# Kernel tuning notes

Measured on AMD Instinct MI355X. Metric: run time of the kernel, lower is better.

## Reference

```python
import jax, jax.numpy as jnp
import numpy as np


def setup_inputs() -> dict:
    key = jax.random.key(0)
    kx, kq, kk, kv = jax.random.split(key, 4)
    d_model, d_head = 1024, 64
    x = jax.random.normal(kx, (4, 4096, d_model), dtype=jnp.float32)
    scale = 1.0 / np.sqrt(d_model)
    Wq = jax.random.normal(kq, (d_model, d_head), dtype=jnp.float32) * scale
    Wk = jax.random.normal(kk, (d_model, d_head), dtype=jnp.float32) * scale
    Wv = jax.random.normal(kv, (d_model, d_head), dtype=jnp.float32) * scale
    return {"x": x, "Wq": Wq, "Wk": Wk, "Wv": Wv}


def reference(x, Wq, Wk, Wv):
    # x: [B, S, D]; Wq/Wk/Wv: [D, H]
    d_head = Wq.shape[-1]
    Q = jnp.einsum('bsd,dh->bsh', x, Wq)
    K = jnp.einsum('bsd,dh->bsh', x, Wk)
    V = jnp.einsum('bsd,dh->bsh', x, Wv)
    scores = jnp.einsum('bqh,bkh->bqk', Q, K) / jnp.sqrt(jnp.float32(d_head))
    S = x.shape[1]
    causal = jnp.tril(jnp.ones((S, S), dtype=bool))  # [S, S]
    scores = jnp.where(causal, scores, -jnp.inf)
    weights = jax.nn.softmax(scores, axis=-1)  # [B, S, S]
    return jnp.einsum('bqk,bkh->bqh', weights, V)
```

## Files before the change

kernel.cpp:

```cpp
#include <hip/hip_runtime.h>

#define D_MODEL 1024
#define D_HEAD  64
#define SEQ     4096
#define BATCH   4
#define M_TOT   (BATCH * SEQ)
#define LOG2E   1.44269504088896f
#define MFIX_L2 17.3123404906676f
#define CHUNK   8

typedef __bf16 bf16;
typedef bf16  bf16x8 __attribute__((ext_vector_type(8)));
typedef bf16  bf16x4v __attribute__((ext_vector_type(4)));
typedef float f32x4  __attribute__((ext_vector_type(4)));

#define MFMA(a, b, c) __builtin_amdgcn_mfma_f32_16x16x32_bf16(a, b, c, 0, 0, 0)

#define QKV_OFF  0
#define OBUF_OFF 6291456
#define LBUF_OFF 10485760
#define WT_OFF   10551296
#define VT_OFF   10944512

__global__ void prep_kernel(const float* __restrict__ Wq, const float* __restrict__ Wk,
                            const float* __restrict__ Wv, bf16* __restrict__ Wt,
                            float4* __restrict__ zp, int n4)
{
    const int bx = blockIdx.x;
    const int t  = threadIdx.x;
    if (bx < 48) {
        __shared__ bf16 tr[64][72];
        const int wm = bx >> 4, kt = bx & 15, k0 = kt * 64;
        const float* W = (wm == 0) ? Wq : (wm == 1) ? Wk : Wv;
        const int kr = t >> 2, nb = (t & 3) * 16;
        #pragma unroll
        for (int j = 0; j < 4; j++) {
            float4 wrow = *(const float4*)(W + (size_t)(k0 + kr) * D_HEAD + nb + j * 4);
            tr[nb + j * 4 + 0][kr] = (bf16)wrow.x;
            tr[nb + j * 4 + 1][kr] = (bf16)wrow.y;
            tr[nb + j * 4 + 2][kr] = (bf16)wrow.z;
            tr[nb + j * 4 + 3][kr] = (bf16)wrow.w;
        }
        __syncthreads();
        const int n = t >> 2, kc = (t & 3) * 8;
        bf16* dst = Wt + (size_t)(wm * 64 + n) * D_MODEL + k0;
        #pragma unroll
        for (int h = 0; h < 2; h++) {
            bf16x8 v;
            #pragma unroll
            for (int j = 0; j < 8; j++) v[j] = tr[n][kc + h * 32 + j];
            *(bf16x8*)(dst + kc + h * 32) = v;
        }
    } else {
        int i = (bx - 48) * 256 + t;
        if (i < n4) zp[i] = float4{0.f, 0.f, 0.f, 0.f};
    }
}

#define XP 40

__global__ __launch_bounds__(512) void proj_kernel(
    const float* __restrict__ x, const bf16* __restrict__ Wt,
    bf16* __restrict__ qkv, bf16* __restrict__ vt)
{
    __shared__ __align__(16) bf16 xs[2][2][64][XP];
    __shared__ __align__(16) bf16 ws[2][2][192][XP];
    __shared__ float red[64][193];

    const int t    = threadIdx.x;
    const int w    = t >> 6;
    const int g    = w >> 2;
    const int nw   = w & 3;
    const int lane = t & 63;
    const int quad = lane >> 4;
    const int l15  = lane & 15;
    const int row0 = blockIdx.x * 64;
    const int kb   = g * 512;

    const int tg   = t & 255;
    const int xrow = tg >> 2, xkq = (tg & 3) * 8;

    const float* xg = x + (size_t)(row0 + xrow) * D_MODEL + kb + xkq;

    f32x4 acc[12] = {};

    float4 xa, xb;
    bf16x8 wtv[3];

    auto load_regs = [&](int c) {
        xa = *(const float4*)(xg + c * 32);
        xb = *(const float4*)(xg + c * 32 + 4);
        #pragma unroll
        for (int it = 0; it < 3; it++) {
            int id = tg + it * 256, n = id >> 2, kk8 = (id & 3) * 8;
            wtv[it] = *(const bf16x8*)(Wt + (size_t)n * D_MODEL + kb + c * 32 + kk8);
        }
    };
    auto store_lds = [&](int p) {
        bf16x8 xv;
        xv[0] = (bf16)xa.x; xv[1] = (bf16)xa.y; xv[2] = (bf16)xa.z; xv[3] = (bf16)xa.w;
        xv[4] = (bf16)xb.x; xv[5] = (bf16)xb.y; xv[6] = (bf16)xb.z; xv[7] = (bf16)xb.w;
        *(bf16x8*)&xs[p][g][xrow][xkq] = xv;
        #pragma unroll
        for (int it = 0; it < 3; it++) {
            int id = tg + it * 256, n = id >> 2, kk8 = (id & 3) * 8;
            *(bf16x8*)&ws[p][g][n][kk8] = wtv[it];
        }
    };

    load_regs(0);
    store_lds(0);
    load_regs(1);
    __syncthreads();

    int p = 0;
    for (int c = 0; c < 16; c++) {
        bf16x8 af[4], bfr[3];
        #pragma unroll
        for (int rg = 0; rg < 4; rg++)
            af[rg] = *(bf16x8*)&xs[p][g][rg * 16 + l15][quad * 8];
        #pragma unroll
        for (int j = 0; j < 3; j++)
            bfr[j] = *(bf16x8*)&ws[p][g][nw * 48 + j * 16 + l15][quad * 8];
        #pragma unroll
        for (int rg = 0; rg < 4; rg++)
            #pragma unroll
            for (int j = 0; j < 3; j++)
                acc[rg * 3 + j] = MFMA(af[rg], bfr[j], acc[rg * 3 + j]);

        if (c + 1 < 16) {
            store_lds(p ^ 1);
            if (c + 2 < 16) load_regs(c + 2);
        }
        __syncthreads();
        p ^= 1;
    }

    if (g == 1) {
        #pragma unroll
        for (int rg = 0; rg < 4; rg++)
            #pragma unroll
            for (int j = 0; j < 3; j++)
                #pragma unroll
                for (int r = 0; r < 4; r++)
                    red[rg * 16 + quad * 4 + r][nw * 48 + j * 16 + l15] =
                        acc[rg * 3 + j][r];
    }
    __syncthreads();
    if (g == 0) {
        const int bb = row0 >> 12, s0 = row0 & (SEQ - 1);
        #pragma unroll
        for (int rg = 0; rg < 4; rg++)
            #pragma unroll
            for (int j = 0; j < 3; j++) {
                const int col = nw * 48 + j * 16 + l15;
                const int wm = col >> 6, h = col & 63;
                if (wm == 2) {
                    bf16x4v vv;
                    #pragma unroll
                    for (int r = 0; r < 4; r++) {
                        const int row = rg * 16 + quad * 4 + r;
                        vv[r] = (bf16)(acc[rg * 3 + j][r] + red[row][col]);
                    }
                    *(bf16x4v*)(vt + ((size_t)bb * D_HEAD + h) * SEQ +
                                s0 + rg * 16 + quad * 4) = vv;
                } else {
                    const float sc = (wm == 0) ? 0.125f : 1.0f;
                    bf16* outp = qkv + (size_t)wm * M_TOT * D_HEAD;
                    #pragma unroll
                    for (int r = 0; r < 4; r++) {
                        const int row = rg * 16 + quad * 4 + r;
                        float s = acc[rg * 3 + j][r] + red[row][col];
                        outp[(size_t)(row0 + row) * D_HEAD + h] = (bf16)(s * sc);
                    }
                }
            }
    }
}

__global__ __launch_bounds__(256, 4) void attn_kernel(
    const bf16* __restrict__ qkv, const bf16* __restrict__ vt,
    float* __restrict__ o_buf, float* __restrict__ l_buf)
{
    const int i = blockIdx.x;
    const int c = blockIdx.y;
    const int b = blockIdx.z;
    const int ntiles = i + 1;
    const int tile0  = c * CHUNK;
    if (tile0 >= ntiles) return;
    const int tile1 = min(tile0 + CHUNK, ntiles);

    __shared__ __align__(16) char KsB[2 * 64 * 128];
    __shared__ __align__(16) char VsB[2 * 64 * 128];

    auto kaddr = [](char* base, int pp, int row, int colb) -> void* {
        return base + pp * 8192 + row * 128 + (colb ^ ((row & 7) << 4));
    };

    const bf16* Q = qkv;
    const bf16* K = qkv + (size_t)M_TOT * D_HEAD;

    const int t    = threadIdx.x;
    const int wv   = t >> 6;
    const int lane = t & 63;
    const int quad = lane >> 4;
    const int l15  = lane & 15;
    const int qb   = i * 64;
    const size_t base  = (size_t)b * SEQ * D_HEAD;
    const bf16* vtb = vt + (size_t)b * D_HEAD * SEQ;

    bf16x8 qf0, qf1;
    {
        const bf16* qr = Q + base + (size_t)(qb + wv * 16 + l15) * D_HEAD;
        qf0 = *(const bf16x8*)(qr + quad * 8);
        qf1 = *(const bf16x8*)(qr + 32 + quad * 8);
    }

    f32x4 o[4] = {};
    float lsum = 0.f;
    const int qw0 = qb + wv * 16;

    const int dr  = t >> 2;
    const int cb  = (t & 3) * 16;

    bf16x8 kr0, kr1, vr0, vr1;
    auto load_kv = [&](int tile) {
        const bf16* kp = K + base + (size_t)(tile * 64 + dr) * D_HEAD;
        kr0 = *(const bf16x8*)(kp + (cb >> 1));
        kr1 = *(const bf16x8*)(kp + (cb >> 1) + 32);
        const bf16* vp = vtb + (size_t)dr * SEQ + tile * 64;
        vr0 = *(const bf16x8*)(vp + (cb >> 1));
        vr1 = *(const bf16x8*)(vp + (cb >> 1) + 32);
    };
    auto store_kv = [&](int pp) {
        *(bf16x8*)kaddr(KsB, pp, dr, cb)      = kr0;
        *(bf16x8*)kaddr(KsB, pp, dr, cb + 64) = kr1;
        *(bf16x8*)kaddr(VsB, pp, dr, cb)      = vr0;
        *(bf16x8*)kaddr(VsB, pp, dr, cb + 64) = vr1;
    };

    load_kv(tile0);
    store_kv(0);
    if (tile0 + 1 < tile1) load_kv(tile0 + 1);
    __syncthreads();

    int p = 0;
    for (int tile = tile0; tile < tile1; tile++) {
        const int kk0 = tile * 64;

        f32x4 sc4[4];
        __builtin_amdgcn_s_setprio(1);
        #pragma unroll
        for (int kt = 0; kt < 4; kt++) {
            f32x4 z = {};
            z = MFMA(*(bf16x8*)kaddr(KsB, p, kt * 16 + l15, quad * 16),      qf0, z);
            z = MFMA(*(bf16x8*)kaddr(KsB, p, kt * 16 + l15, 64 + quad * 16), qf1, z);
            sc4[kt] = z;
        }
        __builtin_amdgcn_s_setprio(0);

        bf16 ph[4][4];
        if (tile == i) {
            #pragma unroll
            for (int kt = 0; kt < 4; kt++)
                #pragma unroll
                for (int r = 0; r < 4; r++) {
                    float s = sc4[kt][r];
                    if (kk0 + kt * 16 + quad * 4 + r > qw0 + l15)
                        s = -1e30f;
                    float pe = __builtin_amdgcn_exp2f(fmaf(s, LOG2E, -MFIX_L2));
                    lsum += pe;
                    ph[kt][r] = (bf16)pe;
                }
        } else {
            #pragma unroll
            for (int kt = 0; kt < 4; kt++)
                #pragma unroll
                for (int r = 0; r < 4; r++) {
                    float pe = __builtin_amdgcn_exp2f(
                        fmaf(sc4[kt][r], LOG2E, -MFIX_L2));
                    lsum += pe;
                    ph[kt][r] = (bf16)pe;
                }
        }

        unsigned pku[4][2];
        #pragma unroll
        for (int kt = 0; kt < 4; kt++) {
            __builtin_memcpy(&pku[kt][0], &ph[kt][0], 4);
            __builtin_memcpy(&pku[kt][1], &ph[kt][2], 4);
        }

        const int srcA = l15 + ((lane & 16) ? 32 : 0);
        const int srcB = srcA + 16;
        const bool hi  = (lane & 32) != 0;

        #pragma unroll
        for (int c2 = 0; c2 < 2; c2++) {
            unsigned xA0 = __shfl((int)pku[2 * c2][0],     srcA);
            unsigned xA1 = __shfl((int)pku[2 * c2][1],     srcA);
            unsigned yA0 = __shfl((int)pku[2 * c2 + 1][0], srcA);
            unsigned yA1 = __shfl((int)pku[2 * c2 + 1][1], srcA);
            unsigned xB0 = __shfl((int)pku[2 * c2][0],     srcB);
            unsigned xB1 = __shfl((int)pku[2 * c2][1],     srcB);
            unsigned yB0 = __shfl((int)pku[2 * c2 + 1][0], srcB);
            unsigned yB1 = __shfl((int)pku[2 * c2 + 1][1], srcB);
            unsigned fr[4];
            fr[0] = hi ? yA0 : xA0;
            fr[1] = hi ? yA1 : xA1;
            fr[2] = hi ? yB0 : xB0;
            fr[3] = hi ? yB1 : xB1;
            bf16x8 pa;
            __builtin_memcpy(&pa, fr, 16);

            __builtin_amdgcn_s_setprio(1);
            #pragma unroll
            for (int t4 = 0; t4 < 4; t4++) {
                bf16x8 vb = *(bf16x8*)kaddr(VsB, p, t4 * 16 + l15,
                                            c2 * 64 + quad * 16);
                o[t4] = MFMA(pa, vb, o[t4]);
            }
            __builtin_amdgcn_s_setprio(0);
        }

        if (tile + 1 < tile1) {
            store_kv(p ^ 1);
            if (tile + 2 < tile1) load_kv(tile + 2);
            __syncthreads();
        }
        p ^= 1;
    }

    const int mrow0 = b * SEQ + qw0;
    lsum += __shfl_xor(lsum, 16, 64);
    lsum += __shfl_xor(lsum, 32, 64);
    if (lane < 16)
        atomicAdd(&l_buf[mrow0 + l15], lsum);
    #pragma unroll
    for (int r = 0; r < 4; r++) {
        const size_t orow = (size_t)(mrow0 + quad * 4 + r) * D_HEAD;
        #pragma unroll
        for (int t4 = 0; t4 < 4; t4++)
            atomicAdd(&o_buf[orow + t4 * 16 + l15], o[t4][r]);
    }
}

__global__ void norm_kernel(const float4* __restrict__ o_buf,
                            const float* __restrict__ l_buf,
                            float4* __restrict__ out)
{
    int gid = blockIdx.x * 256 + threadIdx.x;
    int m = gid >> 4;
    float inv = 1.0f / l_buf[m];
    float4 v = o_buf[gid];
    out[gid] = float4{v.x * inv, v.y * inv, v.z * inv, v.w * inv};
}

extern "C" void kernel_launch(void* const* d_in, const int* in_sizes, int n_in,
                              void* d_out, int out_size, void* d_ws, size_t ws_size,
                              hipStream_t stream) {
    const float* x  = (const float*)d_in[0];
    const float* Wq = (const float*)d_in[1];
    const float* Wk = (const float*)d_in[2];
    const float* Wv = (const float*)d_in[3];

    bf16*  qkv   = (bf16*)((char*)d_ws + QKV_OFF);
    float* o_buf = (float*)((char*)d_ws + OBUF_OFF);
    float* l_buf = (float*)((char*)d_ws + LBUF_OFF);
    bf16*  Wt    = (bf16*)((char*)d_ws + WT_OFF);
    bf16*  vt    = (bf16*)((char*)d_ws + VT_OFF);

    const int zero4 = (M_TOT * 65) / 4;
    const int zblocks = (zero4 + 255) / 256;
    prep_kernel<<<48 + zblocks, 256, 0, stream>>>(Wq, Wk, Wv, Wt,
                                                  (float4*)o_buf, zero4);
    proj_kernel<<<M_TOT / 64, 512, 0, stream>>>(x, Wt, qkv, vt);
    attn_kernel<<<dim3(SEQ / 64, SEQ / 64 / CHUNK, BATCH), 256, 0, stream>>>(
        qkv, vt, o_buf, l_buf);
    norm_kernel<<<M_TOT * 16 / 256, 256, 0, stream>>>((const float4*)o_buf, l_buf,
                                                      (float4*)d_out);
}
```

Measured before the change: 147.8 us.

## Drop split-K in projection, use 32-row tiles, and double attention chunk size

The projection kernel stops splitting the K dimension across two warp groups, which removes the LDS reduction buffer and the extra barrier. It now runs 256-thread blocks over 32-row tiles with a full 1024-wide K loop, giving twice as many blocks. Attention CHUNK grows from 8 to 16, so each block handles more KV tiles and fewer partial outputs get atomically accumulated. In exchange, weight reuse per block drops (each W tile is loaded for only 32 rows), and larger chunks may reduce attention parallelism and load balance.

```diff
diff --git a/kernel.cpp b/kernel.cpp
--- a/kernel.cpp
+++ b/kernel.cpp
@@ -7,7 +7,7 @@
 #define M_TOT   (BATCH * SEQ)
 #define LOG2E   1.44269504088896f
 #define MFIX_L2 17.3123404906676f
-#define CHUNK   8
+#define CHUNK   16
 
 typedef __bf16 bf16;
 typedef bf16  bf16x8 __attribute__((ext_vector_type(8)));
@@ -57,54 +57,47 @@
     }
 }
 
-#define XP 40
-
-__global__ __launch_bounds__(512) void proj_kernel(
+#define PXP 40
+
+__global__ __launch_bounds__(256) void proj_kernel(
     const float* __restrict__ x, const bf16* __restrict__ Wt,
     bf16* __restrict__ qkv, bf16* __restrict__ vt)
 {
-    __shared__ __align__(16) bf16 xs[2][2][64][XP];
-    __shared__ __align__(16) bf16 ws[2][2][192][XP];
-    __shared__ float red[64][193];
+    __shared__ __align__(16) bf16 xs[2][32][PXP];
+    __shared__ __align__(16) bf16 ws[2][192][PXP];
 
     const int t    = threadIdx.x;
-    const int w    = t >> 6;
-    const int g    = w >> 2;
-    const int nw   = w & 3;
+    const int nw   = t >> 6;
     const int lane = t & 63;
     const int quad = lane >> 4;
     const int l15  = lane & 15;
-    const int row0 = blockIdx.x * 64;
-    const int kb   = g * 512;
-
-    const int tg   = t & 255;
-    const int xrow = tg >> 2, xkq = (tg & 3) * 8;
-
-    const float* xg = x + (size_t)(row0 + xrow) * D_MODEL + kb + xkq;
-
-    f32x4 acc[12] = {};
-
-    float4 xa, xb;
+    const int row0 = blockIdx.x * 32;
+
+    const int xrow = t >> 3, xk4 = (t & 7) * 4;
+    const float* xg = x + (size_t)(row0 + xrow) * D_MODEL + xk4;
+
+    f32x4 acc[6] = {};
+
+    float4 xa;
     bf16x8 wtv[3];
 
     auto load_regs = [&](int c) {
         xa = *(const float4*)(xg + c * 32);
-        xb = *(const float4*)(xg + c * 32 + 4);
         #pragma unroll
         for (int it = 0; it < 3; it++) {
-            int id = tg + it * 256, n = id >> 2, kk8 = (id & 3) * 8;
-            wtv[it] = *(const bf16x8*)(Wt + (size_t)n * D_MODEL + kb + c * 32 + kk8);
+            int id = t + it * 256, n = id >> 2, k8 = (id & 3) * 8;
+            wtv[it] = *(const bf16x8*)(Wt + (size_t)n * D_MODEL + c * 32 + k8);
         }
     };
     auto store_lds = [&](int p) {
-        bf16x8 xv;
-        xv[0] = (bf16)xa.x; xv[1] = (bf16)xa.y; xv[2] = (bf16)xa.z; xv[3] = (bf16)xa.w;
-        xv[4] = (bf16)xb.x; xv[5] = (bf16)xb.y; xv[6] = (bf16)xb.z; xv[7] = (bf16)xb.w;
-        *(bf16x8*)&xs[p][g][xrow][xkq] = xv;
+        bf16x4v xv;
+        xv[0] = (bf16)xa.x; xv[1] = (bf16)xa.y;
+        xv[2] = (bf16)xa.z; xv[3] = (bf16)xa.w;
+        *(bf16x4v*)&xs[p][xrow][xk4] = xv;
         #pragma unroll
         for (int it = 0; it < 3; it++) {
-            int id = tg + it * 256, n = id >> 2, kk8 = (id & 3) * 8;
-            *(bf16x8*)&ws[p][g][n][kk8] = wtv[it];
+            int id = t + it * 256, n = id >> 2, k8 = (id & 3) * 8;
+            *(bf16x8*)&ws[p][n][k8] = wtv[it];
         }
     };
 
@@ -114,68 +107,53 @@
     __syncthreads();
 
     int p = 0;
-    for (int c = 0; c < 16; c++) {
-        bf16x8 af[4], bfr[3];
-        #pragma unroll
-        for (int rg = 0; rg < 4; rg++)
-            af[rg] = *(bf16x8*)&xs[p][g][rg * 16 + l15][quad * 8];
+    for (int c = 0; c < 32; c++) {
+        bf16x8 af[2], bfr[3];
+        #pragma unroll
+        for (int rg = 0; rg < 2; rg++)
+            af[rg] = *(bf16x8*)&xs[p][rg * 16 + l15][quad * 8];
         #pragma unroll
         for (int j = 0; j < 3; j++)
-            bfr[j] = *(bf16x8*)&ws[p][g][nw * 48 + j * 16 + l15][quad * 8];
-        #pragma unroll
-        for (int rg = 0; rg < 4; rg++)
+            bfr[j] = *(bf16x8*)&ws[p][nw * 48 + j * 16 + l15][quad * 8];
+        #pragma unroll
+        for (int rg = 0; rg < 2; rg++)
             #pragma unroll
             for (int j = 0; j < 3; j++)
                 acc[rg * 3 + j] = MFMA(af[rg], bfr[j], acc[rg * 3 + j]);
 
-        if (c + 1 < 16) {
+        if (c + 1 < 32) {
             store_lds(p ^ 1);
-            if (c + 2 < 16) load_regs(c + 2);
+            if (c + 2 < 32) load_regs(c + 2);
         }
         __syncthreads();
         p ^= 1;
     }
 
-    if (g == 1) {
-        #pragma unroll
-        for (int rg = 0; rg < 4; rg++)
-            #pragma unroll
-            for (int j = 0; j < 3; j++)
+    const int bb = row0 >> 12, s0 = row0 & (SEQ - 1);
+    #pragma unroll
+    for (int rg = 0; rg < 2; rg++)
+        #pragma unroll
+        for (int j = 0; j < 3; j++) {
+            const int col = nw * 48 + j * 16 + l15;
+            const int wm = col >> 6, h = col & 63;
+            if (wm == 2) {
+                bf16x4v vv;
                 #pragma unroll
                 for (int r = 0; r < 4; r++)
-                    red[rg * 16 + quad * 4 + r][nw * 48 + j * 16 + l15] =
-                        acc[rg * 3 + j][r];
-    }
-    __syncthreads();
-    if (g == 0) {
-        const int bb = row0 >> 12, s0 = row0 & (SEQ - 1);
-        #pragma unroll
-        for (int rg = 0; rg < 4; rg++)
-            #pragma unroll
-            for (int j = 0; j < 3; j++) {
-                const int col = nw * 48 + j * 16 + l15;
-                const int wm = col >> 6, h = col & 63;
-                if (wm == 2) {
-                    bf16x4v vv;
-                    #pragma unroll
-                    for (int r = 0; r < 4; r++) {
-                        const int row = rg * 16 + quad * 4 + r;
-                        vv[r] = (bf16)(acc[rg * 3 + j][r] + red[row][col]);
-                    }
-                    *(bf16x4v*)(vt + ((size_t)bb * D_HEAD + h) * SEQ +
-                                s0 + rg * 16 + quad * 4) = vv;
-                } else {
-                    const float sc = (wm == 0) ? 0.125f : 1.0f;
-                    bf16* outp = qkv + (size_t)wm * M_TOT * D_HEAD;
-                    #pragma unroll
-                    for (int r = 0; r < 4; r++) {
-                        const int row = rg * 16 + quad * 4 + r;
-                        float s = acc[rg * 3 + j][r] + red[row][col];
-                        outp[(size_t)(row0 + row) * D_HEAD + h] = (bf16)(s * sc);
-                    }
+                    vv[r] = (bf16)acc[rg * 3 + j][r];
+                *(bf16x4v*)(vt + ((size_t)bb * D_HEAD + h) * SEQ +
+                            s0 + rg * 16 + quad * 4) = vv;
+            } else {
+                const float sc = (wm == 0) ? 0.125f : 1.0f;
+                bf16* outp = qkv + (size_t)wm * M_TOT * D_HEAD;
+                #pragma unroll
+                for (int r = 0; r < 4; r++) {
+                    const int row = row0 + rg * 16 + quad * 4 + r;
+                    outp[(size_t)row * D_HEAD + h] =
+                        (bf16)(acc[rg * 3 + j][r] * sc);
                 }
             }
-    }
+        }
 }
 
 __global__ __launch_bounds__(256, 4) void attn_kernel(
@@ -374,7 +352,7 @@
     const int zblocks = (zero4 + 255) / 256;
     prep_kernel<<<48 + zblocks, 256, 0, stream>>>(Wq, Wk, Wv, Wt,
                                                   (float4*)o_buf, zero4);
-    proj_kernel<<<M_TOT / 64, 512, 0, stream>>>(x, Wt, qkv, vt);
+    proj_kernel<<<M_TOT / 32, 256, 0, stream>>>(x, Wt, qkv, vt);
     attn_kernel<<<dim3(SEQ / 64, SEQ / 64 / CHUNK, BATCH), 256, 0, stream>>>(
         qkv, vt, o_buf, l_buf);
     norm_kernel<<<M_TOT * 16 / 256, 256, 0, stream>>>((const float4*)o_buf, l_buf,
```

Result: slower. 159.0 us (+7.5%).
